# Optimization experiments

Measured on AMD Instinct MI355X. Metric: run time of the kernel, lower is better.

## Reference

```python
import jax, jax.numpy as jnp
import numpy as np

GRID = 18          # grid_dim
NTYPES = 6         # n_atom_types
SIGMA_P = 0.6      # sigma * bins_per_angstrom
B = 256            # number of environments (batch)
ATOMS_PER_ENV = 100
N = B * ATOMS_PER_ENV
EPS = 1e-5
SLOPE = 0.01       # LeakyReLU default negative slope


def _grid_points():
    # lin_spacing(): centers of 18 unit bins, -8.5 .. 8.5
    ls = np.linspace(-GRID / 2 + 0.5, GRID / 2 - 0.5, GRID)
    xx, yy, zz = np.meshgrid(ls, ls, ls, indexing='ij')
    return jnp.asarray(np.stack([xx, yy, zz], -1).reshape(-1, 3), jnp.float32)  # [G,3]


def _leaky(x):
    return jnp.where(x >= 0, x, SLOPE * x)


def _bn(x, g, b):
    # batch-norm with batch statistics (torch training-mode math), channel axis 1
    axes = tuple(i for i in range(x.ndim) if i != 1)
    m = x.mean(axes, keepdims=True)
    v = x.var(axes, keepdims=True)
    shp = [1] * x.ndim
    shp[1] = -1
    return (x - m) / jnp.sqrt(v + EPS) * g.reshape(shp) + b.reshape(shp)


def _conv3d(x, w, b, pad):
    y = jax.lax.conv_general_dilated(
        x, w, window_strides=(1, 1, 1), padding=[(pad, pad)] * 3,
        dimension_numbers=('NCDHW', 'OIDHW', 'NCDHW'))
    return y + b[None, :, None, None, None]


def _maxpool2(x):
    return jax.lax.reduce_window(x, -jnp.inf, jax.lax.max,
                                 (1, 1, 2, 2, 2), (1, 1, 2, 2, 2), 'VALID')


def _gaussian_blurring(pos, batch_ids, types):
    grid = _grid_points()                                  # [G,3], G=5832
    # squared distances via ||a-b||^2 = ||a||^2 + ||b||^2 - 2 a.b  -> avoids [G,N,3]
    d2 = (jnp.sum(grid * grid, -1)[:, None]
          + jnp.sum(pos * pos, -1)[None, :]
          - 2.0 * grid @ pos.T)                            # [G,N]
    dens = jnp.exp(-d2 / (2.0 * SIGMA_P ** 2))
    dens = dens / jnp.sum(dens, axis=0, keepdims=True)     # normalize per atom
    seg = batch_ids * NTYPES + types                       # [N]
    fields = jax.ops.segment_sum(dens.T, seg, num_segments=B * NTYPES)  # [B*6,G]
    return fields.reshape(B, NTYPES, GRID, GRID, GRID)


def setup_inputs() -> dict:
    key = jax.random.key(0)
    ks = jax.random.split(key, 16)
    pos = jax.random.uniform(ks[0], (N, 3), jnp.float32, -8.5, 8.5)
    batch_ids = jnp.repeat(jnp.arange(B, dtype=jnp.int32), ATOMS_PER_ENV)
    types = (jnp.arange(N, dtype=jnp.int32) % NTYPES)  # every env has every type
    s = 0.05
    return {
        'pos': pos,
        'c1w': jax.random.normal(ks[1], (16, 6, 3, 3, 3), jnp.float32) * s,
        'c1b': jax.random.normal(ks[2], (16,), jnp.float32) * s,
        'bn1g': jnp.ones((16,), jnp.float32), 'bn1b': jnp.zeros((16,), jnp.float32),
        'c2w': jax.random.normal(ks[3], (32, 16, 3, 3, 3), jnp.float32) * s,
        'c2b': jax.random.normal(ks[4], (32,), jnp.float32) * s,
        'bn2g': jnp.ones((32,), jnp.float32), 'bn2b': jnp.zeros((32,), jnp.float32),
        'c3w': jax.random.normal(ks[5], (64, 32, 3, 3, 3), jnp.float32) * s,
        'c3b': jax.random.normal(ks[6], (64,), jnp.float32) * s,
        'bn3g': jnp.ones((64,), jnp.float32), 'bn3b': jnp.zeros((64,), jnp.float32),
        'd1w': jax.random.normal(ks[7], (128, 64), jnp.float32) * s,
        'd1b': jax.random.normal(ks[8], (128,), jnp.float32) * s,
        'bn4g': jnp.ones((128,), jnp.float32), 'bn4b': jnp.zeros((128,), jnp.float32),
        'd2w': jax.random.normal(ks[9], (100, 128), jnp.float32) * s,
        'd2b': jax.random.normal(ks[10], (100,), jnp.float32) * s,
        'd3w': jax.random.normal(ks[11], (20, 100), jnp.float32) * s,
        'd3b': jax.random.normal(ks[12], (20,), jnp.float32) * s,
        'batch_ids': batch_ids,
        'types': types,
    }


def reference(pos, c1w, c1b, bn1g, bn1b, c2w, c2b, bn2g, bn2b, c3w, c3b, bn3g, bn3b,
              d1w, d1b, bn4g, bn4b, d2w, d2b, d3w, d3b, batch_ids, types):
    x = _gaussian_blurring(pos, batch_ids, types)            # [B,6,18,18,18]
    x = _leaky(_bn(_maxpool2(_conv3d(x, c1w, c1b, 1)), bn1g, bn1b))  # [B,16,9,9,9]
    x = _leaky(_bn(_maxpool2(_conv3d(x, c2w, c2b, 0)), bn2g, bn2b))  # [B,32,3,3,3]
    x = _leaky(_bn(_maxpool2(_conv3d(x, c3w, c3b, 1)), bn3g, bn3b))  # [B,64,1,1,1]
    x = x.reshape(x.shape[0], -1)                            # [B,64]
    x = _leaky(_bn(x @ d1w.T + d1b, bn4g, bn4b))             # [B,128]
    x = x @ d2w.T + d2b                                      # [B,100]
    x = _leaky(x)
    x = x @ d3w.T + d3b                                      # [B,20]
    return x
```

## Files before the change

kernel.cpp:

```cpp
#include <hip/hip_runtime.h>


#define G2 324
#define G3 5832
#define NT 6
#define BATCH 256
#define APE 100
#define EPS 1e-5f

typedef unsigned short u16;
typedef unsigned int u32;
typedef _Float16 h2 __attribute__((ext_vector_type(2)));

__device__ __forceinline__ float leaky(float x) { return x >= 0.0f ? x : 0.01f * x; }
__device__ __forceinline__ u32 pkh(float a, float b) {
    h2 v; v[0] = (_Float16)a; v[1] = (_Float16)b;
    return __builtin_bit_cast(u32, v);
}
__device__ __forceinline__ float fdot2u(u32 a, u32 b, float c) {
#if __has_builtin(__builtin_amdgcn_fdot2)
    return __builtin_amdgcn_fdot2(__builtin_bit_cast(h2, a),
                                  __builtin_bit_cast(h2, b), c, false);
#else
    h2 x = __builtin_bit_cast(h2, a), y = __builtin_bit_cast(h2, b);
    return c + (float)x[0] * (float)y[0] + (float)x[1] * (float)y[1];
#endif
}

__global__ __launch_bounds__(512) void k_splat(const float* __restrict__ pos,
        const int* __restrict__ types, u32* __restrict__ fields,
        float* __restrict__ stO) {
    __shared__ float ew[APE * 54];
    __shared__ float ssum[APE * 3];
    __shared__ int list[APE];
    __shared__ int base[NT + 1];
    __shared__ int cnt[NT], cur[NT];
    const int b = blockIdx.x, tid = threadIdx.x;

    if (b == 0 && tid < 480) stO[tid] = 0.0f;
    if (tid < NT) { cnt[tid] = 0; cur[tid] = 0; }
    __syncthreads();
    if (tid < APE) atomicAdd(&cnt[types[b * APE + tid]], 1);
    if (tid < 300) {
        const int la = tid / 3, ax = tid % 3;
        const float p = pos[(b * APE + la) * 3 + ax];
        float s = 0.0f;
        #pragma unroll
        for (int g = 0; g < 18; ++g) {
            const float d = (float)g - 8.5f - p;
            const float e = __expf(d * d * (-1.0f / 0.72f));
            ew[la * 54 + ax * 18 + g] = e;
            s += e;
        }
        ssum[tid] = s;
    }
    __syncthreads();
    if (tid == 0) {
        int s = 0;
        #pragma unroll
        for (int t = 0; t < NT; ++t) { base[t] = s; s += cnt[t]; }
        base[NT] = s;
    }
    if (tid < APE) {
        const float inv = 1.0f / (ssum[tid * 3] * ssum[tid * 3 + 1] * ssum[tid * 3 + 2]);
        #pragma unroll
        for (int g = 0; g < 18; ++g) ew[tid * 54 + g] *= inv;
    }
    __syncthreads();
    if (tid < APE) {
        const int t = types[b * APE + tid];
        const int j = atomicAdd(&cur[t], 1);
        list[base[t] + j] = tid;
    }
    __syncthreads();

    for (int it = tid; it < NT * 324; it += 512) {
        const int t = it / 324, r = it - t * 324;
        const int i = r / 18, j = r % 18;
        float acc[18];
        #pragma unroll
        for (int k = 0; k < 18; ++k) acc[k] = 0.0f;
        const int e1 = base[t + 1];
        for (int u = base[t]; u < e1; ++u) {
            const int a = list[u];
            const float exy = ew[a * 54 + i] * ew[a * 54 + 18 + j];
            const float* ez = &ew[a * 54 + 36];
            #pragma unroll
            for (int k = 0; k < 18; ++k) acc[k] += exy * ez[k];
        }
        u32* dst = &fields[((size_t)b * NT + t) * 2916 + (size_t)r * 9];
        #pragma unroll
        for (int q = 0; q < 9; ++q) dst[q] = pkh(acc[2 * q], acc[2 * q + 1]);
    }
}

template <int ZG>
__device__ __forceinline__ void conv1_pass(int c2, int Xl, int Yv, int b, int Xg,
        const u32* fldH, const u32* wpk, float* s_sum, float* s_ssq,
        const float* __restrict__ bias, float* __restrict__ a1) {
    float acc[2][2][2][6];
    #pragma unroll
    for (int c = 0; c < 2; ++c)
        #pragma unroll
        for (int o = 0; o < 2; ++o)
            #pragma unroll
            for (int p = 0; p < 2; ++p)
                #pragma unroll
                for (int z = 0; z < 6; ++z) acc[c][o][p][z] = 0.0f;

    for (int ic = 0; ic < 6; ++ic) {
        u32 A0[9], A1[9];
        float Bf0[9], Bf1[9];
        #pragma unroll
        for (int d2 = 0; d2 < 9; ++d2) {
            const int wb = ((ic * 9 + d2) * 8 + c2) * 3;
            A0[d2] = wpk[wb]; A1[d2] = wpk[wb + 1];
            const h2 w2 = __builtin_bit_cast(h2, wpk[wb + 2]);
            Bf0[d2] = (float)w2[0]; Bf1[d2] = (float)w2[1];
        }
        #pragma unroll
        for (int lj = 0; lj < 4; ++lj) {
            const int iy = 2 * Yv + lj - 1;
            const bool yok = (iy >= 0 && iy < 18);
            #pragma unroll
            for (int li = 0; li < 4; ++li) {
                const int ixl = 2 * Xl + li;
                u32 V[5], Sh[4];
                if (yok) {
                    const u32* rp = &fldH[((ic * 8 + ixl) * 18 + iy) * 10];
                    if (ZG == 0) {
                        V[0] = 0u;
                        #pragma unroll
                        for (int q = 0; q < 4; ++q) V[q + 1] = rp[q];
                    } else {
                        #pragma unroll
                        for (int q = 0; q < 5; ++q) V[q] = rp[3 * ZG - 1 + q];
                    }
                } else {
                    #pragma unroll
                    for (int q = 0; q < 5; ++q) V[q] = 0u;
                }
                #pragma unroll
                for (int q = 0; q < 4; ++q)
                    Sh[q] = __builtin_amdgcn_alignbit(V[q + 1], V[q], 16);
                float vlo[3], vhi[3];
                #pragma unroll
                for (int q = 0; q < 3; ++q) {
                    const h2 hv = __builtin_bit_cast(h2, V[q + 2]);
                    vlo[q] = (float)hv[0];
                    const h2 hw = __builtin_bit_cast(h2, V[q + 1]);
                    vhi[q] = (float)hw[1];
                }
                #pragma unroll
                for (int o = 0; o < 2; ++o) {
                    const int dx = li - o;
                    if (dx < 0 || dx > 2) continue;
                    #pragma unroll
                    for (int p = 0; p < 2; ++p) {
                        const int dy = lj - p;
                        if (dy < 0 || dy > 2) continue;
                        const int d2 = dx * 3 + dy;
                        #pragma unroll
                        for (int ozl = 0; ozl < 6; ++ozl) {
                            if (ozl & 1) {
                                const int vi = (ozl + 1) >> 1;
                                acc[0][o][p][ozl] = fdot2u(A0[d2], V[vi],
                                    fmaf(Bf0[d2], vlo[vi - 1], acc[0][o][p][ozl]));
                                acc[1][o][p][ozl] = fdot2u(A1[d2], V[vi],
                                    fmaf(Bf1[d2], vlo[vi - 1], acc[1][o][p][ozl]));
                            } else {
                                const int si = ozl >> 1;
                                acc[0][o][p][ozl] = fdot2u(A0[d2], Sh[si],
                                    fmaf(Bf0[d2], vhi[si], acc[0][o][p][ozl]));
                                acc[1][o][p][ozl] = fdot2u(A1[d2], Sh[si],
                                    fmaf(Bf1[d2], vhi[si], acc[1][o][p][ozl]));
                            }
                        }
                    }
                }
            }
        }
    }
    const float bb0 = bias[2 * c2], bb1 = bias[2 * c2 + 1];
    float s0 = 0.0f, q0 = 0.0f, s1 = 0.0f, q1 = 0.0f;
    #pragma unroll
    for (int Zp = 0; Zp < 3; ++Zp) {
        float m0 = acc[0][0][0][2 * Zp], m1 = acc[1][0][0][2 * Zp];
        #pragma unroll
        for (int o = 0; o < 2; ++o)
            #pragma unroll
            for (int p = 0; p < 2; ++p) {
                m0 = fmaxf(m0, fmaxf(acc[0][o][p][2 * Zp], acc[0][o][p][2 * Zp + 1]));
                m1 = fmaxf(m1, fmaxf(acc[1][o][p][2 * Zp], acc[1][o][p][2 * Zp + 1]));
            }
        float2 vv; vv.x = m0 + bb0; vv.y = m1 + bb1;
        s0 += vv.x; q0 += vv.x * vv.x; s1 += vv.y; q1 += vv.y * vv.y;
        const int spg = (3 * Xg + Xl) * 81 + Yv * 9 + 3 * ZG + Zp;
        *(float2*)&a1[((size_t)b * 729 + spg) * 16 + 2 * c2] = vv;
    }
    atomicAdd(&s_sum[2 * c2], s0);     atomicAdd(&s_ssq[2 * c2], q0);
    atomicAdd(&s_sum[2 * c2 + 1], s1); atomicAdd(&s_ssq[2 * c2 + 1], q1);
}

__global__ __launch_bounds__(256, 3) void k_conv1(const u32* __restrict__ fields,
        const float* __restrict__ w, const float* __restrict__ bias,
        float* __restrict__ a1, float* __restrict__ stO) {
    __shared__ u32 fldH[48 * 18 * 10];
    __shared__ u32 wpk[432 * 3];
    __shared__ float s_sum[16], s_ssq[16];
    const int bx = blockIdx.x, b = bx / 3, Xg = bx % 3, tid = threadIdx.x;

    for (int i = tid; i < 432; i += 256) {
        const int c2 = i & 7, t = i >> 3, d2 = t % 9, ic = t / 9;
        const int w0 = (2 * c2) * 162 + ic * 27 + d2 * 3;
        const int w1 = w0 + 162;
        wpk[i * 3]     = pkh(w[w0], w[w0 + 1]);
        wpk[i * 3 + 1] = pkh(w[w1], w[w1 + 1]);
        wpk[i * 3 + 2] = pkh(w[w0 + 2], w[w1 + 2]);
    }
    if (tid < 16) { s_sum[tid] = 0.0f; s_ssq[tid] = 0.0f; }
    for (int i = tid; i < 8640; i += 256) {
        const int p = i % 10, t = i / 10;
        const int iy = t % 18, a = t / 18;
        const int ix = 6 * Xg - 1 + (a & 7);
        u32 v = 0;
        if (p < 9 && ix >= 0 && ix < 18)
            v = fields[((size_t)(b * 6 + (a >> 3)) * 324 + ix * 18 + iy) * 9 + p];
        fldH[t * 10 + p] = v;
    }
    __syncthreads();

    const int c2 = tid & 7, sp = tid >> 3;
    if (tid < 216) {
        const int Xl = sp / 9, Yv = sp % 9;
        conv1_pass<0>(c2, Xl, Yv, b, Xg, fldH, wpk, s_sum, s_ssq, bias, a1);
        conv1_pass<1>(c2, Xl, Yv, b, Xg, fldH, wpk, s_sum, s_ssq, bias, a1);
        conv1_pass<2>(c2, Xl, Yv, b, Xg, fldH, wpk, s_sum, s_ssq, bias, a1);
    }
    __syncthreads();
    if (tid < 16) { atomicAdd(&stO[tid], s_sum[tid]); atomicAdd(&stO[16 + tid], s_ssq[tid]); }
}

__global__ __launch_bounds__(320) void k_conv2(const float* __restrict__ a1,
        const float* __restrict__ w, const float* __restrict__ bias,
        const float* __restrict__ bng, const float* __restrict__ bnb,
        const float* __restrict__ stI, float* __restrict__ a2,
        float* __restrict__ stO) {
    __shared__ float xin[16 * 729];
    __shared__ float ws2[6912];
    __shared__ float sc[16], sh[16];
    __shared__ float s_sum[16], s_ssq[16];
    const int bx = blockIdx.x, b = bx >> 1, half = bx & 1, tid = threadIdx.x;
    if (tid < 16) {
        const float cnt = 256.0f * 729.0f;
        float m = stI[tid] / cnt;
        float v = stI[16 + tid] / cnt - m * m;
        float s = bng[tid] * rsqrtf(fmaxf(v, 0.0f) + EPS);
        sc[tid] = s; sh[tid] = bnb[tid] - m * s;
        s_sum[tid] = 0.0f; s_ssq[tid] = 0.0f;
    }
    __syncthreads();
    const float* src = a1 + (size_t)b * 729 * 16;
    for (int i = tid; i < 16 * 729; i += 320) {
        const int spb = i >> 4, c = i & 15;
        xin[c * 729 + spb] = leaky(src[i] * sc[c] + sh[c]);
    }
    for (int i = tid; i < 6912; i += 320) ws2[i] = w[half * 6912 + i];
    __syncthreads();
    if (tid < 288) {
        const int oyi = tid & 1, oxi = (tid >> 1) & 1, rest = tid >> 2;
        const int Y = rest % 3, X = (rest / 3) % 3, c2 = rest / 9;
        const int ox = 2 * X + oxi, oy = 2 * Y + oyi;
        const int cl0 = 2 * c2, cl1 = cl0 + 1;
        float acc0[6], acc1[6];
        #pragma unroll
        for (int z = 0; z < 6; ++z) { acc0[z] = 0.0f; acc1[z] = 0.0f; }
        for (int ic = 0; ic < 16; ++ic) {
            #pragma unroll
            for (int dx = 0; dx < 3; ++dx) {
                const int ix = ox + dx;
                #pragma unroll
                for (int dy = 0; dy < 3; ++dy) {
                    const int iy = oy + dy;
                    const float* rp = &xin[ic * 729 + ix * 81 + iy * 9];
                    float row[9];
                    #pragma unroll
                    for (int z = 0; z < 9; ++z) row[z] = rp[z];
                    const int wb0 = (cl0 * 16 + ic) * 27 + dx * 9 + dy * 3;
                    const int wb1 = (cl1 * 16 + ic) * 27 + dx * 9 + dy * 3;
                    #pragma unroll
                    for (int dz = 0; dz < 3; ++dz) {
                        const float w0 = ws2[wb0 + dz];
                        const float w1v = ws2[wb1 + dz];
                        #pragma unroll
                        for (int z = 0; z < 6; ++z) {
                            acc0[z] += w0 * row[z + dz];
                            acc1[z] += w1v * row[z + dz];
                        }
                    }
                }
            }
        }
        float pl[2][3];
        #pragma unroll
        for (int Z = 0; Z < 3; ++Z) {
            float v0 = fmaxf(acc0[2 * Z], acc0[2 * Z + 1]);
            float v1 = fmaxf(acc1[2 * Z], acc1[2 * Z + 1]);
            v0 = fmaxf(v0, __shfl_xor(v0, 1)); v0 = fmaxf(v0, __shfl_xor(v0, 2));
            v1 = fmaxf(v1, __shfl_xor(v1, 1)); v1 = fmaxf(v1, __shfl_xor(v1, 2));
            pl[0][Z] = v0; pl[1][Z] = v1;
        }
        if ((tid & 3) == 0) {
            #pragma unroll
            for (int hh = 0; hh < 2; ++hh) {
                const int cl = cl0 + hh, c = half * 16 + cl;
                const float bb = bias[c];
                float s0 = 0.0f, q0 = 0.0f;
                #pragma unroll
                for (int Z = 0; Z < 3; ++Z) {
                    const float v = pl[hh][Z] + bb;
                    a2[((size_t)b * 32 + c) * 27 + X * 9 + Y * 3 + Z] = v;
                    s0 += v; q0 += v * v;
                }
                atomicAdd(&s_sum[cl], s0); atomicAdd(&s_ssq[cl], q0);
            }
        }
    }
    __syncthreads();
    if (tid < 16) {
        const int c = half * 16 + tid;
        atomicAdd(&stO[c], s_sum[tid]); atomicAdd(&stO[32 + c], s_ssq[tid]);
    }
}

__global__ __launch_bounds__(256) void k_conv3(const float* __restrict__ a2,
        const float* __restrict__ w, const float* __restrict__ bias,
        const float* __restrict__ bng, const float* __restrict__ bnb,
        const float* __restrict__ stI, float* __restrict__ a3,
        float* __restrict__ stO) {
    __shared__ float x[864];
    __shared__ float pacc[256 * 8];
    __shared__ float sc[32], sh[32];
    const int b = blockIdx.x, tid = threadIdx.x;
    if (tid < 32) {
        const float cnt = 256.0f * 27.0f;
        float m = stI[tid] / cnt;
        float v = stI[32 + tid] / cnt - m * m;
        float s = bng[tid] * rsqrtf(fmaxf(v, 0.0f) + EPS);
        sc[tid] = s; sh[tid] = bnb[tid] - m * s;
    }
    __syncthreads();
    for (int i = tid; i < 864; i += 256) {
        int c = i / 27;
        x[i] = leaky(a2[(size_t)b * 864 + i] * sc[c] + sh[c]);
    }
    __syncthreads();
    const int c = tid & 63, q = tid >> 6;
    float acc[8];
    #pragma unroll
    for (int p = 0; p < 8; ++p) acc[p] = 0.0f;
    for (int ic = q * 8; ic < q * 8 + 8; ++ic) {
        const float* wr = w + ((size_t)c * 32 + ic) * 27;
        #pragma unroll
        for (int d = 0; d < 27; ++d) {
            const int dx = d / 9, dy = (d / 3) % 3, dz = d % 3;
            const float wv = wr[d];
            #pragma unroll
            for (int p = 0; p < 8; ++p) {
                const int px = p >> 2, py = (p >> 1) & 1, pz = p & 1;
                const int ix = px + dx - 1, iy = py + dy - 1, iz = pz + dz - 1;
                if (ix >= 0 && iy >= 0 && iz >= 0)
                    acc[p] += wv * x[ic * 27 + ix * 9 + iy * 3 + iz];
            }
        }
    }
    #pragma unroll
    for (int p = 0; p < 8; ++p) pacc[tid * 8 + p] = acc[p];
    __syncthreads();
    if (q == 0) {
        float m = -1e30f;
        #pragma unroll
        for (int p = 0; p < 8; ++p) {
            float v = pacc[c * 8 + p] + pacc[(64 + c) * 8 + p]
                    + pacc[(128 + c) * 8 + p] + pacc[(192 + c) * 8 + p];
            m = fmaxf(m, v);
        }
        float v = m + bias[c];
        a3[(size_t)b * 64 + c] = v;
        atomicAdd(&stO[c], v); atomicAdd(&stO[64 + c], v * v);
    }
}

__global__ __launch_bounds__(128) void k_dense1(const float* __restrict__ a3,
        const float* __restrict__ bng, const float* __restrict__ bnb,
        const float* __restrict__ stI,
        const float* __restrict__ w1, const float* __restrict__ b1,
        float* __restrict__ h1, float* __restrict__ stO) {
    __shared__ float x[64];
    const int b = blockIdx.x, tid = threadIdx.x;
    if (tid < 64) {
        float m = stI[tid] / 256.0f;
        float v = stI[64 + tid] / 256.0f - m * m;
        float s = bng[tid] * rsqrtf(fmaxf(v, 0.0f) + EPS);
        x[tid] = leaky(a3[(size_t)b * 64 + tid] * s + (bnb[tid] - m * s));
    }
    __syncthreads();
    const float* wr = w1 + tid * 64;
    float acc = b1[tid];
    #pragma unroll
    for (int i = 0; i < 64; ++i) acc += x[i] * wr[i];
    h1[(size_t)b * 128 + tid] = acc;
    atomicAdd(&stO[tid], acc); atomicAdd(&stO[128 + tid], acc * acc);
}

__global__ __launch_bounds__(128) void k_dense2(const float* __restrict__ h1,
        const float* __restrict__ bng, const float* __restrict__ bnb,
        const float* __restrict__ stI,
        const float* __restrict__ w2, const float* __restrict__ bias2,
        const float* __restrict__ w3, const float* __restrict__ bias3,
        float* __restrict__ out) {
    __shared__ float x[128];
    __shared__ float y[100];
    const int b = blockIdx.x, tid = threadIdx.x;
    {
        float m = stI[tid] / 256.0f;
        float v = stI[128 + tid] / 256.0f - m * m;
        float s = bng[tid] * rsqrtf(fmaxf(v, 0.0f) + EPS);
        x[tid] = leaky(h1[(size_t)b * 128 + tid] * s + (bnb[tid] - m * s));
    }
    __syncthreads();
    if (tid < 100) {
        const float* wr = w2 + tid * 128;
        float acc = bias2[tid];
        #pragma unroll
        for (int i = 0; i < 128; ++i) acc += x[i] * wr[i];
        y[tid] = leaky(acc);
    }
    __syncthreads();
    if (tid < 20) {
        const float* wr = w3 + tid * 100;
        float acc = bias3[tid];
        #pragma unroll
        for (int i = 0; i < 100; ++i) acc += y[i] * wr[i];
        out[(size_t)b * 20 + tid] = acc;
    }
}

extern "C" void kernel_launch(void* const* d_in, const int* in_sizes, int n_in,
                              void* d_out, int out_size, void* d_ws, size_t ws_size,
                              hipStream_t stream) {
    (void)in_sizes; (void)n_in; (void)out_size; (void)ws_size;
    const float* pos  = (const float*)d_in[0];
    const float* c1w  = (const float*)d_in[1];
    const float* c1b  = (const float*)d_in[2];
    const float* bn1g = (const float*)d_in[3];
    const float* bn1b = (const float*)d_in[4];
    const float* c2w  = (const float*)d_in[5];
    const float* c2b  = (const float*)d_in[6];
    const float* bn2g = (const float*)d_in[7];
    const float* bn2b = (const float*)d_in[8];
    const float* c3w  = (const float*)d_in[9];
    const float* c3b  = (const float*)d_in[10];
    const float* bn3g = (const float*)d_in[11];
    const float* bn3b = (const float*)d_in[12];
    const float* d1w  = (const float*)d_in[13];
    const float* d1b  = (const float*)d_in[14];
    const float* bn4g = (const float*)d_in[15];
    const float* bn4b = (const float*)d_in[16];
    const float* d2w  = (const float*)d_in[17];
    const float* d2b  = (const float*)d_in[18];
    const float* d3w  = (const float*)d_in[19];
    const float* d3b  = (const float*)d_in[20];
    const int* types  = (const int*)d_in[22];

    float* ws = (float*)d_ws;
    float* st = ws;
    float* a3 = ws + 512;
    float* h1 = a3 + 16384;
    float* a2 = h1 + 32768;
    float* a1 = a2 + 221184;
    u32* fields = (u32*)(a1 + 2985984);

    k_splat <<<BATCH, 512, 0, stream>>>(pos, types, fields, st);
    k_conv1 <<<3 * BATCH, 256, 0, stream>>>(fields, c1w, c1b, a1, st);
    k_conv2 <<<2 * BATCH, 320, 0, stream>>>(a1, c2w, c2b, bn1g, bn1b, st, a2, st + 32);
    k_conv3 <<<BATCH, 256, 0, stream>>>(a2, c3w, c3b, bn2g, bn2b, st + 32, a3, st + 96);
    k_dense1<<<BATCH, 128, 0, stream>>>(a3, bn3g, bn3b, st + 96, d1w, d1b, h1, st + 224);
    k_dense2<<<BATCH, 128, 0, stream>>>(h1, bn4g, bn4b, st + 224, d2w, d2b, d3w, d3b,
                                        (float*)d_out);
}
```

Baseline: 241.5 us.

## Fuse conv2, conv3 and dense layers into one persistent kernel with grid barriers

Replaces the four tail kernels with a single kernel that keeps one block per batch element. Intermediates stay in shared memory, and the batch-norm statistics are synchronised through atomic-counter grid barriers instead of separate launches. This removes three kernel launches and the global round-trips for a2, a3 and h1. In exchange, conv2 now runs in one 512-thread block per sample instead of two blocks, which lowers parallelism and raises shared-memory use. The barriers also assume all 256 blocks are resident at once, so the kernel deadlocks if they are not.

```diff
diff --git a/kernel.cpp b/kernel.cpp
--- a/kernel.cpp
+++ b/kernel.cpp
@@ -26,10 +26,23 @@
     return c + (float)x[0] * (float)y[0] + (float)x[1] * (float)y[1];
 #endif
 }
+__device__ __forceinline__ float ldst(const float* p) {
+    return __hip_atomic_load(p, __ATOMIC_RELAXED, __HIP_MEMORY_SCOPE_AGENT);
+}
+__device__ __forceinline__ void gbar(int* c, int n) {
+    __syncthreads();
+    if (threadIdx.x == 0) {
+        __threadfence();
+        __hip_atomic_fetch_add(c, 1, __ATOMIC_ACQ_REL, __HIP_MEMORY_SCOPE_AGENT);
+        while (__hip_atomic_load(c, __ATOMIC_ACQUIRE, __HIP_MEMORY_SCOPE_AGENT) < n)
+            __builtin_amdgcn_s_sleep(8);
+    }
+    __syncthreads();
+}
 
 __global__ __launch_bounds__(512) void k_splat(const float* __restrict__ pos,
         const int* __restrict__ types, u32* __restrict__ fields,
-        float* __restrict__ stO) {
+        float* __restrict__ stO, int* __restrict__ ctr) {
     __shared__ float ew[APE * 54];
     __shared__ float ssum[APE * 3];
     __shared__ int list[APE];
@@ -38,6 +51,7 @@
     const int b = blockIdx.x, tid = threadIdx.x;
 
     if (b == 0 && tid < 480) stO[tid] = 0.0f;
+    if (b == 0 && tid >= 480 && tid < 484) ctr[tid - 480] = 0;
     if (tid < NT) { cnt[tid] = 0; cur[tid] = 0; }
     __syncthreads();
     if (tid < APE) atomicAdd(&cnt[types[b * APE + tid]], 1);
@@ -241,37 +255,48 @@
     if (tid < 16) { atomicAdd(&stO[tid], s_sum[tid]); atomicAdd(&stO[16 + tid], s_ssq[tid]); }
 }
 
-__global__ __launch_bounds__(320) void k_conv2(const float* __restrict__ a1,
-        const float* __restrict__ w, const float* __restrict__ bias,
-        const float* __restrict__ bng, const float* __restrict__ bnb,
-        const float* __restrict__ stI, float* __restrict__ a2,
-        float* __restrict__ stO) {
+__global__ __launch_bounds__(512) void k_tail(const float* __restrict__ a1,
+        const float* __restrict__ w2c, const float* __restrict__ b2c,
+        const float* __restrict__ bn1g, const float* __restrict__ bn1b,
+        const float* __restrict__ w3c, const float* __restrict__ b3c,
+        const float* __restrict__ bn2g, const float* __restrict__ bn2b,
+        const float* __restrict__ d1w, const float* __restrict__ d1b,
+        const float* __restrict__ bn3g, const float* __restrict__ bn3b,
+        const float* __restrict__ d2w, const float* __restrict__ d2b,
+        const float* __restrict__ bn4g, const float* __restrict__ bn4b,
+        const float* __restrict__ d3w, const float* __restrict__ d3b,
+        float* __restrict__ st, int* __restrict__ ctr,
+        float* __restrict__ out) {
     __shared__ float xin[16 * 729];
-    __shared__ float ws2[6912];
-    __shared__ float sc[16], sh[16];
-    __shared__ float s_sum[16], s_ssq[16];
-    const int bx = blockIdx.x, b = bx >> 1, half = bx & 1, tid = threadIdx.x;
+    __shared__ float ws2[13824];
+    __shared__ float a2l[864];
+    __shared__ float x3[864];
+    __shared__ float pacc[512 * 8];
+    __shared__ float a3l[64], h1l[128], xc[128], yv[100];
+    __shared__ float sc[32], sh[32], s_sum[32], s_ssq[32];
+    const int b = blockIdx.x, tid = threadIdx.x;
+
     if (tid < 16) {
-        const float cnt = 256.0f * 729.0f;
-        float m = stI[tid] / cnt;
-        float v = stI[16 + tid] / cnt - m * m;
-        float s = bng[tid] * rsqrtf(fmaxf(v, 0.0f) + EPS);
-        sc[tid] = s; sh[tid] = bnb[tid] - m * s;
-        s_sum[tid] = 0.0f; s_ssq[tid] = 0.0f;
-    }
+        const float cntc = 256.0f * 729.0f;
+        float m = st[tid] / cntc;
+        float v = st[16 + tid] / cntc - m * m;
+        float s = bn1g[tid] * rsqrtf(fmaxf(v, 0.0f) + EPS);
+        sc[tid] = s; sh[tid] = bn1b[tid] - m * s;
+    }
+    if (tid < 32) { s_sum[tid] = 0.0f; s_ssq[tid] = 0.0f; }
     __syncthreads();
     const float* src = a1 + (size_t)b * 729 * 16;
-    for (int i = tid; i < 16 * 729; i += 320) {
+    for (int i = tid; i < 16 * 729; i += 512) {
         const int spb = i >> 4, c = i & 15;
         xin[c * 729 + spb] = leaky(src[i] * sc[c] + sh[c]);
     }
-    for (int i = tid; i < 6912; i += 320) ws2[i] = w[half * 6912 + i];
-    __syncthreads();
-    if (tid < 288) {
-        const int oyi = tid & 1, oxi = (tid >> 1) & 1, rest = tid >> 2;
+    for (int i = tid; i < 13824; i += 512) ws2[i] = w2c[i];
+    __syncthreads();
+    for (int idx = tid; idx < 576; idx += 512) {
+        const int oyi = idx & 1, oxi = (idx >> 1) & 1, rest = idx >> 2;
         const int Y = rest % 3, X = (rest / 3) % 3, c2 = rest / 9;
         const int ox = 2 * X + oxi, oy = 2 * Y + oyi;
-        const int cl0 = 2 * c2, cl1 = cl0 + 1;
+        const int c0 = 2 * c2, c1 = c0 + 1;
         float acc0[6], acc1[6];
         #pragma unroll
         for (int z = 0; z < 6; ++z) { acc0[z] = 0.0f; acc1[z] = 0.0f; }
@@ -286,8 +311,8 @@
                     float row[9];
                     #pragma unroll
                     for (int z = 0; z < 9; ++z) row[z] = rp[z];
-                    const int wb0 = (cl0 * 16 + ic) * 27 + dx * 9 + dy * 3;
-                    const int wb1 = (cl1 * 16 + ic) * 27 + dx * 9 + dy * 3;
+                    const int wb0 = (c0 * 16 + ic) * 27 + dx * 9 + dy * 3;
+                    const int wb1 = (c1 * 16 + ic) * 27 + dx * 9 + dy * 3;
                     #pragma unroll
                     for (int dz = 0; dz < 3; ++dz) {
                         const float w0 = ws2[wb0 + dz];
@@ -310,138 +335,116 @@
             v1 = fmaxf(v1, __shfl_xor(v1, 1)); v1 = fmaxf(v1, __shfl_xor(v1, 2));
             pl[0][Z] = v0; pl[1][Z] = v1;
         }
-        if ((tid & 3) == 0) {
+        if ((idx & 3) == 0) {
             #pragma unroll
             for (int hh = 0; hh < 2; ++hh) {
-                const int cl = cl0 + hh, c = half * 16 + cl;
-                const float bb = bias[c];
+                const int c = c0 + hh;
+                const float bb = b2c[c];
                 float s0 = 0.0f, q0 = 0.0f;
                 #pragma unroll
                 for (int Z = 0; Z < 3; ++Z) {
                     const float v = pl[hh][Z] + bb;
-                    a2[((size_t)b * 32 + c) * 27 + X * 9 + Y * 3 + Z] = v;
+                    a2l[c * 27 + X * 9 + Y * 3 + Z] = v;
                     s0 += v; q0 += v * v;
                 }
-                atomicAdd(&s_sum[cl], s0); atomicAdd(&s_ssq[cl], q0);
+                atomicAdd(&s_sum[c], s0); atomicAdd(&s_ssq[c], q0);
             }
         }
     }
     __syncthreads();
-    if (tid < 16) {
-        const int c = half * 16 + tid;
-        atomicAdd(&stO[c], s_sum[tid]); atomicAdd(&stO[32 + c], s_ssq[tid]);
-    }
-}
-
-__global__ __launch_bounds__(256) void k_conv3(const float* __restrict__ a2,
-        const float* __restrict__ w, const float* __restrict__ bias,
-        const float* __restrict__ bng, const float* __restrict__ bnb,
-        const float* __restrict__ stI, float* __restrict__ a3,
-        float* __restrict__ stO) {
-    __shared__ float x[864];
-    __shared__ float pacc[256 * 8];
-    __shared__ float sc[32], sh[32];
-    const int b = blockIdx.x, tid = threadIdx.x;
+    if (tid < 32) { atomicAdd(&st[32 + tid], s_sum[tid]); atomicAdd(&st[64 + tid], s_ssq[tid]); }
+    gbar(&ctr[0], BATCH);
+
     if (tid < 32) {
-        const float cnt = 256.0f * 27.0f;
-        float m = stI[tid] / cnt;
-        float v = stI[32 + tid] / cnt - m * m;
-        float s = bng[tid] * rsqrtf(fmaxf(v, 0.0f) + EPS);
-        sc[tid] = s; sh[tid] = bnb[tid] - m * s;
-    }
-    __syncthreads();
-    for (int i = tid; i < 864; i += 256) {
-        int c = i / 27;
-        x[i] = leaky(a2[(size_t)b * 864 + i] * sc[c] + sh[c]);
-    }
-    __syncthreads();
-    const int c = tid & 63, q = tid >> 6;
-    float acc[8];
-    #pragma unroll
-    for (int p = 0; p < 8; ++p) acc[p] = 0.0f;
-    for (int ic = q * 8; ic < q * 8 + 8; ++ic) {
-        const float* wr = w + ((size_t)c * 32 + ic) * 27;
-        #pragma unroll
-        for (int d = 0; d < 27; ++d) {
-            const int dx = d / 9, dy = (d / 3) % 3, dz = d % 3;
-            const float wv = wr[d];
-            #pragma unroll
-            for (int p = 0; p < 8; ++p) {
-                const int px = p >> 2, py = (p >> 1) & 1, pz = p & 1;
-                const int ix = px + dx - 1, iy = py + dy - 1, iz = pz + dz - 1;
-                if (ix >= 0 && iy >= 0 && iz >= 0)
-                    acc[p] += wv * x[ic * 27 + ix * 9 + iy * 3 + iz];
+        const float cntc = 256.0f * 27.0f;
+        float m = ldst(&st[32 + tid]) / cntc;
+        float v = ldst(&st[64 + tid]) / cntc - m * m;
+        float s = bn2g[tid] * rsqrtf(fmaxf(v, 0.0f) + EPS);
+        sc[tid] = s; sh[tid] = bn2b[tid] - m * s;
+    }
+    __syncthreads();
+    for (int i = tid; i < 864; i += 512) {
+        const int c = i / 27;
+        x3[i] = leaky(a2l[i] * sc[c] + sh[c]);
+    }
+    __syncthreads();
+    {
+        const int c = tid & 63, q = tid >> 6;
+        float acc[8];
+        #pragma unroll
+        for (int p = 0; p < 8; ++p) acc[p] = 0.0f;
+        for (int ic = q * 4; ic < q * 4 + 4; ++ic) {
+            const float* wr = w3c + ((size_t)c * 32 + ic) * 27;
+            #pragma unroll
+            for (int d = 0; d < 27; ++d) {
+                const int dx = d / 9, dy = (d / 3) % 3, dz = d % 3;
+                const float wv = wr[d];
+                #pragma unroll
+                for (int p = 0; p < 8; ++p) {
+                    const int px = p >> 2, py = (p >> 1) & 1, pz = p & 1;
+                    const int ix = px + dx - 1, iy = py + dy - 1, iz = pz + dz - 1;
+                    if (ix >= 0 && iy >= 0 && iz >= 0)
+                        acc[p] += wv * x3[ic * 27 + ix * 9 + iy * 3 + iz];
+                }
             }
         }
-    }
-    #pragma unroll
-    for (int p = 0; p < 8; ++p) pacc[tid * 8 + p] = acc[p];
-    __syncthreads();
-    if (q == 0) {
+        #pragma unroll
+        for (int p = 0; p < 8; ++p) pacc[tid * 8 + p] = acc[p];
+    }
+    __syncthreads();
+    if (tid < 64) {
+        const int c = tid;
         float m = -1e30f;
         #pragma unroll
         for (int p = 0; p < 8; ++p) {
-            float v = pacc[c * 8 + p] + pacc[(64 + c) * 8 + p]
-                    + pacc[(128 + c) * 8 + p] + pacc[(192 + c) * 8 + p];
+            float v = 0.0f;
+            #pragma unroll
+            for (int qq = 0; qq < 8; ++qq) v += pacc[(qq * 64 + c) * 8 + p];
             m = fmaxf(m, v);
         }
-        float v = m + bias[c];
-        a3[(size_t)b * 64 + c] = v;
-        atomicAdd(&stO[c], v); atomicAdd(&stO[64 + c], v * v);
-    }
-}
-
-__global__ __launch_bounds__(128) void k_dense1(const float* __restrict__ a3,
-        const float* __restrict__ bng, const float* __restrict__ bnb,
-        const float* __restrict__ stI,
-        const float* __restrict__ w1, const float* __restrict__ b1,
-        float* __restrict__ h1, float* __restrict__ stO) {
-    __shared__ float x[64];
-    const int b = blockIdx.x, tid = threadIdx.x;
+        const float v = m + b3c[c];
+        a3l[c] = v;
+        atomicAdd(&st[96 + c], v); atomicAdd(&st[160 + c], v * v);
+    }
+    gbar(&ctr[1], BATCH);
+
     if (tid < 64) {
-        float m = stI[tid] / 256.0f;
-        float v = stI[64 + tid] / 256.0f - m * m;
-        float s = bng[tid] * rsqrtf(fmaxf(v, 0.0f) + EPS);
-        x[tid] = leaky(a3[(size_t)b * 64 + tid] * s + (bnb[tid] - m * s));
-    }
-    __syncthreads();
-    const float* wr = w1 + tid * 64;
-    float acc = b1[tid];
-    #pragma unroll
-    for (int i = 0; i < 64; ++i) acc += x[i] * wr[i];
-    h1[(size_t)b * 128 + tid] = acc;
-    atomicAdd(&stO[tid], acc); atomicAdd(&stO[128 + tid], acc * acc);
-}
-
-__global__ __launch_bounds__(128) void k_dense2(const float* __restrict__ h1,
-        const float* __restrict__ bng, const float* __restrict__ bnb,
-        const float* __restrict__ stI,
-        const float* __restrict__ w2, const float* __restrict__ bias2,
-        const float* __restrict__ w3, const float* __restrict__ bias3,
-        float* __restrict__ out) {
-    __shared__ float x[128];
-    __shared__ float y[100];
-    const int b = blockIdx.x, tid = threadIdx.x;
-    {
-        float m = stI[tid] / 256.0f;
-        float v = stI[128 + tid] / 256.0f - m * m;
-        float s = bng[tid] * rsqrtf(fmaxf(v, 0.0f) + EPS);
-        x[tid] = leaky(h1[(size_t)b * 128 + tid] * s + (bnb[tid] - m * s));
+        float m = ldst(&st[96 + tid]) / 256.0f;
+        float v = ldst(&st[160 + tid]) / 256.0f - m * m;
+        float s = bn3g[tid] * rsqrtf(fmaxf(v, 0.0f) + EPS);
+        xc[tid] = leaky(a3l[tid] * s + (bn3b[tid] - m * s));
+    }
+    __syncthreads();
+    if (tid < 128) {
+        const float* wr = d1w + tid * 64;
+        float acc = d1b[tid];
+        #pragma unroll
+        for (int i = 0; i < 64; ++i) acc += xc[i] * wr[i];
+        h1l[tid] = acc;
+        atomicAdd(&st[224 + tid], acc); atomicAdd(&st[352 + tid], acc * acc);
+    }
+    gbar(&ctr[2], BATCH);
+
+    if (tid < 128) {
+        float m = ldst(&st[224 + tid]) / 256.0f;
+        float v = ldst(&st[352 + tid]) / 256.0f - m * m;
+        float s = bn4g[tid] * rsqrtf(fmaxf(v, 0.0f) + EPS);
+        xc[tid] = leaky(h1l[tid] * s + (bn4b[tid] - m * s));
     }
     __syncthreads();
     if (tid < 100) {
-        const float* wr = w2 + tid * 128;
-        float acc = bias2[tid];
-        #pragma unroll
-        for (int i = 0; i < 128; ++i) acc += x[i] * wr[i];
-        y[tid] = leaky(acc);
+        const float* wr = d2w + tid * 128;
+        float acc = d2b[tid];
+        #pragma unroll
+        for (int i = 0; i < 128; ++i) acc += xc[i] * wr[i];
+        yv[tid] = leaky(acc);
     }
     __syncthreads();
     if (tid < 20) {
-        const float* wr = w3 + tid * 100;
-        float acc = bias3[tid];
-        #pragma unroll
-        for (int i = 0; i < 100; ++i) acc += y[i] * wr[i];
+        const float* wr = d3w + tid * 100;
+        float acc = d3b[tid];
+        #pragma unroll
+        for (int i = 0; i < 100; ++i) acc += yv[i] * wr[i];
         out[(size_t)b * 20 + tid] = acc;
     }
 }
@@ -475,17 +478,14 @@
 
     float* ws = (float*)d_ws;
     float* st = ws;
-    float* a3 = ws + 512;
-    float* h1 = a3 + 16384;
-    float* a2 = h1 + 32768;
-    float* a1 = a2 + 221184;
+    int* ctr = (int*)(ws + 480);
+    float* a1 = ws + 512;
     u32* fields = (u32*)(a1 + 2985984);
 
-    k_splat <<<BATCH, 512, 0, stream>>>(pos, types, fields, st);
+    k_splat <<<BATCH, 512, 0, stream>>>(pos, types, fields, st, ctr);
     k_conv1 <<<3 * BATCH, 256, 0, stream>>>(fields, c1w, c1b, a1, st);
-    k_conv2 <<<2 * BATCH, 320, 0, stream>>>(a1, c2w, c2b, bn1g, bn1b, st, a2, st + 32);
-    k_conv3 <<<BATCH, 256, 0, stream>>>(a2, c3w, c3b, bn2g, bn2b, st + 32, a3, st + 96);
-    k_dense1<<<BATCH, 128, 0, stream>>>(a3, bn3g, bn3b, st + 96, d1w, d1b, h1, st + 224);
-    k_dense2<<<BATCH, 128, 0, stream>>>(h1, bn4g, bn4b, st + 224, d2w, d2b, d3w, d3b,
-                                        (float*)d_out);
-}
+    k_tail  <<<BATCH, 512, 0, stream>>>(a1, c2w, c2b, bn1g, bn1b, c3w, c3b,
+                                        bn2g, bn2b, d1w, d1b, bn3g, bn3b,
+                                        d2w, d2b, bn4g, bn4b, d3w, d3b,
+                                        st, ctr, (float*)d_out);
+}
```

Measured after the change: 269.6 us. 1.12x slower.
